# Kernel optimization log

Hardware: AMD Instinct MI355X
Metric: run time of the kernel (lower is better)

## Reference

```python
import jax, jax.numpy as jnp
import numpy as np

N_NODES = 200000
N_EVENTS = 200000
MEM_DIM = 128
MSG_DIM = 128
TIME_DIM = 16
MSG_IN = 2 * MEM_DIM + MSG_DIM + TIME_DIM  # 400


def setup_inputs() -> dict:
    key = jax.random.key(0)
    ks = jax.random.split(key, 12)
    return {
        "src_ids": jax.random.randint(ks[0], (N_EVENTS,), 0, N_NODES, dtype=jnp.int32),
        "dst_ids": jax.random.randint(ks[1], (N_EVENTS,), 0, N_NODES, dtype=jnp.int32),
        "edge_feat": jax.random.normal(ks[2], (N_EVENTS, MSG_DIM), dtype=jnp.float32),
        "timestamps": jax.random.uniform(ks[3], (N_EVENTS,), dtype=jnp.float32),
        "memory": jax.random.normal(ks[4], (N_NODES, MEM_DIM), dtype=jnp.float32) * 0.1,
        "last_update_time": jnp.zeros((N_NODES,), dtype=jnp.float32),
        "time_w": jax.random.normal(ks[5], (TIME_DIM,), dtype=jnp.float32),
        "time_phi": jnp.zeros((TIME_DIM,), dtype=jnp.float32),
        "W1": jax.random.normal(ks[6], (MSG_IN, MSG_DIM), dtype=jnp.float32) / np.sqrt(MSG_IN),
        "b1": jnp.zeros((MSG_DIM,), dtype=jnp.float32),
        "W2": jax.random.normal(ks[7], (MSG_DIM, MSG_DIM), dtype=jnp.float32) / np.sqrt(MSG_DIM),
        "b2": jnp.zeros((MSG_DIM,), dtype=jnp.float32),
        "W_ih": jax.random.normal(ks[8], (3 * MEM_DIM, MSG_DIM), dtype=jnp.float32) / np.sqrt(MSG_DIM),
        "W_hh": jax.random.normal(ks[9], (3 * MEM_DIM, MEM_DIM), dtype=jnp.float32) / np.sqrt(MEM_DIM),
        "b_ih": jnp.zeros((3 * MEM_DIM,), dtype=jnp.float32),
        "b_hh": jnp.zeros((3 * MEM_DIM,), dtype=jnp.float32),
    }


def _time_encode(dt, w, phi):
    # Time2Vec: linear first channel, sin on the rest
    wt = dt[:, None] * w[None, :] + phi[None, :]  # [E, TIME_DIM]
    return jnp.concatenate([wt[:, :1], jnp.sin(wt[:, 1:])], axis=-1)


def _message_mlp(x, W1, b1, W2, b2):
    h = jax.nn.relu(x @ W1 + b1)
    return h @ W2 + b2


def _gru_cell(x, h, W_ih, W_hh, b_ih, b_hh):
    gi = x @ W_ih.T + b_ih  # [U, 3H]
    gh = h @ W_hh.T + b_hh
    i_r, i_z, i_n = jnp.split(gi, 3, axis=-1)
    h_r, h_z, h_n = jnp.split(gh, 3, axis=-1)
    r = jax.nn.sigmoid(i_r + h_r)
    z = jax.nn.sigmoid(i_z + h_z)
    n = jnp.tanh(i_n + r * h_n)
    return (1.0 - z) * n + z * h


def reference(src_ids, dst_ids, edge_feat, timestamps, memory, last_update_time,
              time_w, time_phi, W1, b1, W2, b2, W_ih, W_hh, b_ih, b_hh):
    # 1) gather + time encode
    dt_src = timestamps - last_update_time[src_ids]
    dt_dst = timestamps - last_update_time[dst_ids]
    te_src = _time_encode(dt_src, time_w, time_phi)
    te_dst = _time_encode(dt_dst, time_w, time_phi)
    src_mem = memory[src_ids]
    dst_mem = memory[dst_ids]

    # 2) messages
    msg_src = _message_mlp(jnp.concatenate([src_mem, dst_mem, edge_feat, te_src], -1), W1, b1, W2, b2)
    msg_dst = _message_mlp(jnp.concatenate([dst_mem, src_mem, edge_feat, te_dst], -1), W1, b1, W2, b2)

    all_nodes = jnp.concatenate([src_ids, dst_ids])  # [2E]
    all_msgs = jnp.concatenate([msg_src, msg_dst], axis=0)  # [2E, MSG_DIM]

    # 3) 'last' aggregation: segment-max of positions, then gather
    pos = jnp.arange(all_nodes.shape[0], dtype=jnp.int32)
    last_pos = jax.ops.segment_max(pos, all_nodes, num_segments=N_NODES)  # int32 min where absent
    present = last_pos >= 0  # [N]
    agg = all_msgs[jnp.clip(last_pos, 0, None)]  # [N, MSG_DIM]
    agg = jnp.where(present[:, None], agg, 0.0)

    # 4) GRU memory update on involved nodes only
    new_mem = _gru_cell(agg, memory, W_ih, W_hh, b_ih, b_hh)
    memory_out = jnp.where(present[:, None], new_mem, memory)
    return memory_out
```

## Files before the change

kernel.cpp:

```cpp
#include <hip/hip_runtime.h>
#include <hip/hip_bf16.h>
#include <math.h>

#define NN 200000
#define NE 200000

typedef __attribute__((ext_vector_type(8))) short bf16x8;
typedef __attribute__((ext_vector_type(4))) float f32x4;

#define XASTR 136
#define XBSTR 296
#define OSTR  132
#define NT    (NN / 32)
#define PBT   (32 * XBSTR)

__device__ __forceinline__ float sigm(float x) { return 1.0f / (1.0f + __expf(-x)); }
__device__ __forceinline__ float tanh_f(float x) {
    float e = __expf(2.0f * x);
    return 1.0f - 2.0f / (e + 1.0f);
}
__device__ __forceinline__ ushort f2b(float x) {
    union { __hip_bfloat16 b; ushort u; } v;
    v.b = __float2bfloat16(x);
    return v.u;
}
__device__ __forceinline__ float b2f(ushort u) {
    return __uint_as_float(((unsigned)u) << 16);
}
__device__ __forceinline__ ushort4 cvt4(float4 v) {
    ushort4 u; u.x = f2b(v.x); u.y = f2b(v.y); u.z = f2b(v.z); u.w = f2b(v.w);
    return u;
}
__device__ __forceinline__ void gload_lds16(const ushort* g, ushort* l) {
    __builtin_amdgcn_global_load_lds(
        (const __attribute__((address_space(1))) unsigned int*)g,
        (__attribute__((address_space(3))) unsigned int*)l, 16, 0, 0);
}

#define MFMA16(a, b, c) __builtin_amdgcn_mfma_f32_16x16x32_bf16((a), (b), (c), 0, 0, 0)

#define NB_PREP 594
#define NB_SCAT (((2 * NE) + 255) / 256)
__global__ void k_pre(const float* __restrict__ W1, const float* __restrict__ W2,
                      const float* __restrict__ Wih, const float* __restrict__ Whh,
                      const float* __restrict__ b2, const float* __restrict__ bih,
                      ushort* __restrict__ W1F, ushort* __restrict__ W2IF,
                      ushort* __restrict__ WHF, float* __restrict__ cb,
                      const int* __restrict__ src, const int* __restrict__ dst,
                      int* __restrict__ last_pos) {
    int b = blockIdx.x;
    if (b >= NB_PREP) {
        int i = (b - NB_PREP) * 256 + threadIdx.x;
        if (i < NE) {
            atomicMax(&last_pos[src[i]], i);
        } else if (i < 2 * NE) {
            atomicMax(&last_pos[dst[i - NE]], i);
        }
        return;
    }
    int t = b * 256 + threadIdx.x;
    if (t < 104 * 512) {
        int f = t >> 9, idx = t & 511;
        int lane = idx >> 3, j = idx & 7, c16 = lane & 15, k8 = lane >> 4;
        int wvv = f / 26, r = f % 26, kt = r >> 1, ns = r & 1;
        int col = wvv * 32 + ns * 16 + c16;
        int kk = kt * 32 + k8 * 8 + j;
        W1F[t] = (kk < 400) ? f2b(W1[kk * 128 + col]) : (ushort)0;
        return;
    }
    t -= 104 * 512;
    if (t < 96 * 512) {
        int f = t >> 9, idx = t & 511;
        int lane = idx >> 3, j = idx & 7, c16 = lane & 15, k8 = lane >> 4;
        int wvv = f / 24, r = f % 24, kt = r / 6, rem = r % 6, g = rem >> 1, ns = rem & 1;
        int col = g * 128 + wvv * 32 + ns * 16 + c16;
        int kk = kt * 32 + k8 * 8 + j;
        float s = 0.0f;
        for (int c = 0; c < 128; ++c) s = fmaf(W2[kk * 128 + c], Wih[col * 128 + c], s);
        W2IF[f * 512 + idx] = f2b(s);
        return;
    }
    t -= 96 * 512;
    if (t < 96 * 512) {
        int f = t >> 9, idx = t & 511;
        int lane = idx >> 3, j = idx & 7, c16 = lane & 15, k8 = lane >> 4;
        int wvv = f / 24, r = f % 24, kt = r / 6, rem = r % 6, g = rem >> 1, ns = rem & 1;
        int col = g * 128 + wvv * 32 + ns * 16 + c16;
        int kk = kt * 32 + k8 * 8 + j;
        WHF[f * 512 + idx] = f2b(Whh[col * 128 + kk]);
        return;
    }
    t -= 96 * 512;
    if (t < 384) {
        float s = bih[t];
        for (int k = 0; k < 128; ++k) s = fmaf(b2[k], Wih[t * 128 + k], s);
        cb[t] = s;
    }
}

__global__ __launch_bounds__(256)
void k_gath(const int* __restrict__ last_pos,
            const int* __restrict__ src, const int* __restrict__ dst,
            const float* __restrict__ ts, const float* __restrict__ lut,
            const float* __restrict__ mem, const float* __restrict__ ef,
            const float* __restrict__ tw, const float* __restrict__ tphi,
            ushort* __restrict__ PB)
{
    const int wv = threadIdx.x >> 6, lane = threadIdx.x & 63;
    const int n0 = (blockIdx.x * 4 + wv) * 4;
    const int l = lane & 31;
    const bool lo = lane < 32;

    int p[4];
    #pragma unroll
    for (int s = 0; s < 4; ++s) p[s] = last_pos[n0 + s];

    float4 mv[4], fv[4];
    float te[4];
    #pragma unroll
    for (int s = 0; s < 4; ++s) {
        te[s] = 0.0f;
        if (p[s] >= 0) {
            int e = (p[s] < NE) ? p[s] : p[s] - NE;
            int o = (p[s] < NE) ? dst[e] : src[e];
            if (lo) {
                mv[s] = *(const float4*)&mem[(size_t)o * 128 + l * 4];
                if (l < 16) {
                    float dt = ts[e] - lut[n0 + s];
                    float w = fmaf(dt, tw[l], tphi[l]);
                    te[s] = (l == 0) ? w : __sinf(w);
                }
            } else {
                fv[s] = *(const float4*)&ef[(size_t)e * 128 + l * 4];
            }
        }
    }
    #pragma unroll
    for (int s = 0; s < 4; ++s) {
        if (p[s] >= 0) {
            ushort* xb = PB + (size_t)(n0 + s) * XBSTR;
            if (lo) {
                *(ushort4*)&xb[l * 4] = cvt4(mv[s]);
                xb[256 + l] = (l < 16) ? f2b(te[s]) : (ushort)0;
            } else {
                *(ushort4*)&xb[128 + l * 4] = cvt4(fv[s]);
            }
        }
    }
}

__global__ __launch_bounds__(256, 3)
void k_main8(const ushort* __restrict__ PB, const int* __restrict__ last_pos,
             const float* __restrict__ mem,
             const ushort* __restrict__ W1F, const float* __restrict__ b1,
             const ushort* __restrict__ W2IF, const ushort* __restrict__ WHF,
             const float* __restrict__ cb, const float* __restrict__ bhh,
             float* __restrict__ out)
{
    __shared__ __align__(16) ushort XA[32 * XASTR];
    __shared__ __align__(16) ushort HB[32 * XASTR];
    __shared__ __align__(16) ushort XB[32 * XBSTR];
    __shared__ unsigned char pres[32];

    const int tile = (NT - 1) - blockIdx.x;
    const int base = tile * 32;
    const int tid  = threadIdx.x;
    const int lane = tid & 63;
    const int wv   = tid >> 6;
    const int r16  = lane & 15;
    const int kb   = lane >> 4;

    {
        const ushort* srcPB = PB + (size_t)tile * PBT;
        #pragma unroll
        for (int j = 0; j < 5; ++j) {
            int cc = wv + j * 4;
            if (cc < 18) gload_lds16(srcPB + cc * 512 + lane * 8, XB + cc * 512);
            else if (cc == 18 && lane < 32) gload_lds16(srcPB + cc * 512 + lane * 8, XB + cc * 512);
        }
    }
    {
        const float* msrc = mem + (size_t)base * 128;
        #pragma unroll
        for (int k = 0; k < 4; ++k) {
            int i0 = k * 1024 + tid * 4;
            float4 v = *(const float4*)&msrc[i0];
            *(ushort4*)&XA[(i0 >> 7) * XASTR + (i0 & 127)] = cvt4(v);
        }
        if (tid < 32) pres[tid] = (unsigned char)(last_pos[base + tid] >= 0);
    }
    const ushort* w1 = W1F  + wv * (26 * 512) + lane * 8;
    const ushort* wI = W2IF + wv * (24 * 512) + lane * 8;
    const ushort* wH = WHF  + wv * (24 * 512) + lane * 8;
    __syncthreads();

    f32x4 c1[2][2] = {};
    {
        const ushort* aA = &XA[r16 * XASTR + kb * 8];
        const ushort* aB = &XB[r16 * XBSTR + kb * 8];
        __builtin_amdgcn_s_setprio(1);
        #pragma unroll
        for (int kt = 0; kt < 13; ++kt) {
            const ushort* ap  = (kt < 4) ? (aA + kt * 32) : (aB + (kt - 4) * 32);
            const int     ast = (kt < 4) ? XASTR : XBSTR;
            bf16x8 A0 = *(const bf16x8*)ap;
            bf16x8 A1 = *(const bf16x8*)(ap + 16 * ast);
            bf16x8 B0 = *(const bf16x8*)(w1 + (kt * 2 + 0) * 512);
            bf16x8 B1 = *(const bf16x8*)(w1 + (kt * 2 + 1) * 512);
            c1[0][0] = MFMA16(A0, B0, c1[0][0]);
            c1[0][1] = MFMA16(A0, B1, c1[0][1]);
            c1[1][0] = MFMA16(A1, B0, c1[1][0]);
            c1[1][1] = MFMA16(A1, B1, c1[1][1]);
        }
        __builtin_amdgcn_s_setprio(0);
    }
    #pragma unroll
    for (int ns = 0; ns < 2; ++ns) {
        int col = wv * 32 + ns * 16 + r16;
        float bb = b1[col];
        #pragma unroll
        for (int m = 0; m < 2; ++m)
            #pragma unroll
            for (int r = 0; r < 4; ++r)
                HB[(m * 16 + kb * 4 + r) * XASTR + col] =
                    f2b(fmaxf(c1[m][ns][r] + bb, 0.0f));
    }
    __syncthreads();

    f32x4 arz[2][4] = {};
    f32x4 an_i[2][2] = {};
    f32x4 an_h[2][2] = {};
    {
        const ushort* am = &HB[r16 * XASTR + kb * 8];
        const ushort* ah = &XA[r16 * XASTR + kb * 8];
        __builtin_amdgcn_s_setprio(1);
        #pragma unroll
        for (int kt = 0; kt < 4; ++kt) {
            bf16x8 M0 = *(const bf16x8*)(am + kt * 32);
            bf16x8 M1 = *(const bf16x8*)(am + 16 * XASTR + kt * 32);
            bf16x8 H0 = *(const bf16x8*)(ah + kt * 32);
            bf16x8 H1 = *(const bf16x8*)(ah + 16 * XASTR + kt * 32);
            #pragma unroll
            for (int g = 0; g < 2; ++g)
                #pragma unroll
                for (int ns = 0; ns < 2; ++ns) {
                    int fo = (kt * 6 + g * 2 + ns) * 512;
                    bf16x8 Bi = *(const bf16x8*)(wI + fo);
                    bf16x8 Bh = *(const bf16x8*)(wH + fo);
                    arz[0][g * 2 + ns] = MFMA16(M0, Bi, arz[0][g * 2 + ns]);
                    arz[0][g * 2 + ns] = MFMA16(H0, Bh, arz[0][g * 2 + ns]);
                    arz[1][g * 2 + ns] = MFMA16(M1, Bi, arz[1][g * 2 + ns]);
                    arz[1][g * 2 + ns] = MFMA16(H1, Bh, arz[1][g * 2 + ns]);
                }
            #pragma unroll
            for (int ns = 0; ns < 2; ++ns) {
                int fo = (kt * 6 + 4 + ns) * 512;
                bf16x8 Bi = *(const bf16x8*)(wI + fo);
                bf16x8 Bh = *(const bf16x8*)(wH + fo);
                an_i[0][ns] = MFMA16(M0, Bi, an_i[0][ns]);
                an_i[1][ns] = MFMA16(M1, Bi, an_i[1][ns]);
                an_h[0][ns] = MFMA16(H0, Bh, an_h[0][ns]);
                an_h[1][ns] = MFMA16(H1, Bh, an_h[1][ns]);
            }
        }
        __builtin_amdgcn_s_setprio(0);
    }

    float* XBf = (float*)XB;
    #pragma unroll
    for (int ns = 0; ns < 2; ++ns) {
        int col = wv * 32 + ns * 16 + r16;
        float brz0 = cb[col] + bhh[col];
        float brz1 = cb[128 + col] + bhh[128 + col];
        float bin  = cb[256 + col];
        float bhn  = bhh[256 + col];
        #pragma unroll
        for (int m = 0; m < 2; ++m) {
            #pragma unroll
            for (int r = 0; r < 4; ++r) {
                int row = m * 16 + kb * 4 + r;
                float rr = sigm(arz[m][0 + ns][r] + brz0);
                float zz = sigm(arz[m][2 + ns][r] + brz1);
                float nn = tanh_f(an_i[m][ns][r] + bin +
                                  rr * (an_h[m][ns][r] + bhn));
                float hh = b2f(XA[row * XASTR + col]);
                XBf[row * OSTR + col] = (1.0f - zz) * nn + zz * hh;
            }
        }
    }
    __syncthreads();

    for (int j = wv; j < 32; j += 4) {
        float2 v;
        if (pres[j]) v = *(const float2*)&XBf[j * OSTR + lane * 2];
        else         v = *(const float2*)&mem[(size_t)(base + j) * 128 + lane * 2];
        *(float2*)&out[(size_t)(base + j) * 128 + lane * 2] = v;
    }
}

extern "C" void kernel_launch(void* const* d_in, const int* in_sizes, int n_in,
                              void* d_out, int out_size, void* d_ws, size_t ws_size,
                              hipStream_t stream) {
    const int*   src  = (const int*)d_in[0];
    const int*   dst  = (const int*)d_in[1];
    const float* ef   = (const float*)d_in[2];
    const float* ts   = (const float*)d_in[3];
    const float* mem  = (const float*)d_in[4];
    const float* lut  = (const float*)d_in[5];
    const float* tw   = (const float*)d_in[6];
    const float* tphi = (const float*)d_in[7];
    const float* W1   = (const float*)d_in[8];
    const float* b1   = (const float*)d_in[9];
    const float* W2   = (const float*)d_in[10];
    const float* b2   = (const float*)d_in[11];
    const float* Wih  = (const float*)d_in[12];
    const float* Whh  = (const float*)d_in[13];
    const float* bih  = (const float*)d_in[14];
    const float* bhh  = (const float*)d_in[15];
    float* out = (float*)d_out;

    char* ws = (char*)d_ws;
    size_t off = 0;
    int*    last_pos = (int*)(ws + off);    off += (size_t)NN * 4;
    ushort* W1F      = (ushort*)(ws + off); off += (size_t)104 * 512 * 2;
    ushort* W2IF     = (ushort*)(ws + off); off += (size_t)96 * 512 * 2;
    ushort* WHF      = (ushort*)(ws + off); off += (size_t)96 * 512 * 2;
    float*  cb       = (float*)(ws + off);  off += (size_t)384 * 4 + 64;
    ushort* PB       = (ushort*)(ws + off);

    hipMemsetAsync(last_pos, 0xFF, (size_t)NN * sizeof(int), stream);

    k_pre<<<NB_PREP + NB_SCAT, 256, 0, stream>>>(
        W1, W2, Wih, Whh, b2, bih, W1F, W2IF, WHF, cb, src, dst, last_pos);
    k_gath<<<NN / 16, 256, 0, stream>>>(last_pos, src, dst, ts, lut, mem, ef, tw, tphi, PB);
    k_main8<<<NT, 256, 0, stream>>>(PB, last_pos, mem, W1F, b1, W2IF, WHF, cb, bhh, out);
}
```

Before: 260.3 us.

## Regroup kernels: split scatter out, fuse weight prep with gather, raise occupancy

```diff
diff --git a/kernel.cpp b/kernel.cpp
--- a/kernel.cpp
+++ b/kernel.cpp
@@ -39,75 +39,76 @@
 
 #define MFMA16(a, b, c) __builtin_amdgcn_mfma_f32_16x16x32_bf16((a), (b), (c), 0, 0, 0)
 
+__global__ void k_scatter(const int* __restrict__ src, const int* __restrict__ dst,
+                          int* __restrict__ last_pos) {
+    int i = blockIdx.x * blockDim.x + threadIdx.x;
+    if (i < NE) {
+        atomicMax(&last_pos[src[i]], i);
+    } else if (i < 2 * NE) {
+        atomicMax(&last_pos[dst[i - NE]], i);
+    }
+}
+
 #define NB_PREP 594
-#define NB_SCAT (((2 * NE) + 255) / 256)
-__global__ void k_pre(const float* __restrict__ W1, const float* __restrict__ W2,
-                      const float* __restrict__ Wih, const float* __restrict__ Whh,
-                      const float* __restrict__ b2, const float* __restrict__ bih,
-                      ushort* __restrict__ W1F, ushort* __restrict__ W2IF,
-                      ushort* __restrict__ WHF, float* __restrict__ cb,
-                      const int* __restrict__ src, const int* __restrict__ dst,
-                      int* __restrict__ last_pos) {
+#define NB_GATH (NN / 16)
+__global__ __launch_bounds__(256)
+void k_pg(const float* __restrict__ W1, const float* __restrict__ W2,
+          const float* __restrict__ Wih, const float* __restrict__ Whh,
+          const float* __restrict__ b2, const float* __restrict__ bih,
+          ushort* __restrict__ W1F, ushort* __restrict__ W2IF,
+          ushort* __restrict__ WHF, float* __restrict__ cb,
+          const int* __restrict__ last_pos,
+          const int* __restrict__ src, const int* __restrict__ dst,
+          const float* __restrict__ ts, const float* __restrict__ lut,
+          const float* __restrict__ mem, const float* __restrict__ ef,
+          const float* __restrict__ tw, const float* __restrict__ tphi,
+          ushort* __restrict__ PB)
+{
     int b = blockIdx.x;
-    if (b >= NB_PREP) {
-        int i = (b - NB_PREP) * 256 + threadIdx.x;
-        if (i < NE) {
-            atomicMax(&last_pos[src[i]], i);
-        } else if (i < 2 * NE) {
-            atomicMax(&last_pos[dst[i - NE]], i);
+    if (b < NB_PREP) {
+        int t = b * 256 + threadIdx.x;
+        if (t < 104 * 512) {
+            int f = t >> 9, idx = t & 511;
+            int lane = idx >> 3, j = idx & 7, c16 = lane & 15, k8 = lane >> 4;
+            int wvv = f / 26, r = f % 26, kt = r >> 1, ns = r & 1;
+            int col = wvv * 32 + ns * 16 + c16;
+            int kk = kt * 32 + k8 * 8 + j;
+            W1F[t] = (kk < 400) ? f2b(W1[kk * 128 + col]) : (ushort)0;
+            return;
+        }
+        t -= 104 * 512;
+        if (t < 96 * 512) {
+            int f = t >> 9, idx = t & 511;
+            int lane = idx >> 3, j = idx & 7, c16 = lane & 15, k8 = lane >> 4;
+            int wvv = f / 24, r = f % 24, kt = r / 6, rem = r % 6, g = rem >> 1, ns = rem & 1;
+            int col = g * 128 + wvv * 32 + ns * 16 + c16;
+            int kk = kt * 32 + k8 * 8 + j;
+            float s = 0.0f;
+            for (int c = 0; c < 128; ++c) s = fmaf(W2[kk * 128 + c], Wih[col * 128 + c], s);
+            W2IF[f * 512 + idx] = f2b(s);
+            return;
+        }
+        t -= 96 * 512;
+        if (t < 96 * 512) {
+            int f = t >> 9, idx = t & 511;
+            int lane = idx >> 3, j = idx & 7, c16 = lane & 15, k8 = lane >> 4;
+            int wvv = f / 24, r = f % 24, kt = r / 6, rem = r % 6, g = rem >> 1, ns = rem & 1;
+            int col = g * 128 + wvv * 32 + ns * 16 + c16;
+            int kk = kt * 32 + k8 * 8 + j;
+            WHF[f * 512 + idx] = f2b(Whh[col * 128 + kk]);
+            return;
+        }
+        t -= 96 * 512;
+        if (t < 384) {
+            float s = bih[t];
+            for (int k = 0; k < 128; ++k) s = fmaf(b2[k], Wih[t * 128 + k], s);
+            cb[t] = s;
         }
         return;
     }
-    int t = b * 256 + threadIdx.x;
-    if (t < 104 * 512) {
-        int f = t >> 9, idx = t & 511;
-        int lane = idx >> 3, j = idx & 7, c16 = lane & 15, k8 = lane >> 4;
-        int wvv = f / 26, r = f % 26, kt = r >> 1, ns = r & 1;
-        int col = wvv * 32 + ns * 16 + c16;
-        int kk = kt * 32 + k8 * 8 + j;
-        W1F[t] = (kk < 400) ? f2b(W1[kk * 128 + col]) : (ushort)0;
-        return;
-    }
-    t -= 104 * 512;
-    if (t < 96 * 512) {
-        int f = t >> 9, idx = t & 511;
-        int lane = idx >> 3, j = idx & 7, c16 = lane & 15, k8 = lane >> 4;
-        int wvv = f / 24, r = f % 24, kt = r / 6, rem = r % 6, g = rem >> 1, ns = rem & 1;
-        int col = g * 128 + wvv * 32 + ns * 16 + c16;
-        int kk = kt * 32 + k8 * 8 + j;
-        float s = 0.0f;
-        for (int c = 0; c < 128; ++c) s = fmaf(W2[kk * 128 + c], Wih[col * 128 + c], s);
-        W2IF[f * 512 + idx] = f2b(s);
-        return;
-    }
-    t -= 96 * 512;
-    if (t < 96 * 512) {
-        int f = t >> 9, idx = t & 511;
-        int lane = idx >> 3, j = idx & 7, c16 = lane & 15, k8 = lane >> 4;
-        int wvv = f / 24, r = f % 24, kt = r / 6, rem = r % 6, g = rem >> 1, ns = rem & 1;
-        int col = g * 128 + wvv * 32 + ns * 16 + c16;
-        int kk = kt * 32 + k8 * 8 + j;
-        WHF[f * 512 + idx] = f2b(Whh[col * 128 + kk]);
-        return;
-    }
-    t -= 96 * 512;
-    if (t < 384) {
-        float s = bih[t];
-        for (int k = 0; k < 128; ++k) s = fmaf(b2[k], Wih[t * 128 + k], s);
-        cb[t] = s;
-    }
-}
-
-__global__ __launch_bounds__(256)
-void k_gath(const int* __restrict__ last_pos,
-            const int* __restrict__ src, const int* __restrict__ dst,
-            const float* __restrict__ ts, const float* __restrict__ lut,
-            const float* __restrict__ mem, const float* __restrict__ ef,
-            const float* __restrict__ tw, const float* __restrict__ tphi,
-            ushort* __restrict__ PB)
-{
+
     const int wv = threadIdx.x >> 6, lane = threadIdx.x & 63;
-    const int n0 = (blockIdx.x * 4 + wv) * 4;
+    const int n0 = (((b - NB_PREP) * 4) + wv) * 4;
     const int l = lane & 31;
     const bool lo = lane < 32;
 
@@ -149,8 +150,8 @@
     }
 }
 
-__global__ __launch_bounds__(256, 3)
-void k_main8(const ushort* __restrict__ PB, const int* __restrict__ last_pos,
+__global__ __launch_bounds__(256, 4)
+void k_main9(const ushort* __restrict__ PB, const int* __restrict__ last_pos,
              const float* __restrict__ mem,
              const ushort* __restrict__ W1F, const float* __restrict__ b1,
              const ushort* __restrict__ W2IF, const ushort* __restrict__ WHF,
@@ -198,7 +199,6 @@
     {
         const ushort* aA = &XA[r16 * XASTR + kb * 8];
         const ushort* aB = &XB[r16 * XBSTR + kb * 8];
-        __builtin_amdgcn_s_setprio(1);
         #pragma unroll
         for (int kt = 0; kt < 13; ++kt) {
             const ushort* ap  = (kt < 4) ? (aA + kt * 32) : (aB + (kt - 4) * 32);
@@ -212,7 +212,6 @@
             c1[1][0] = MFMA16(A1, B0, c1[1][0]);
             c1[1][1] = MFMA16(A1, B1, c1[1][1]);
         }
-        __builtin_amdgcn_s_setprio(0);
     }
     #pragma unroll
     for (int ns = 0; ns < 2; ++ns) {
@@ -233,7 +232,6 @@
     {
         const ushort* am = &HB[r16 * XASTR + kb * 8];
         const ushort* ah = &XA[r16 * XASTR + kb * 8];
-        __builtin_amdgcn_s_setprio(1);
         #pragma unroll
         for (int kt = 0; kt < 4; ++kt) {
             bf16x8 M0 = *(const bf16x8*)(am + kt * 32);
@@ -263,7 +261,6 @@
                 an_h[1][ns] = MFMA16(H1, Bh, an_h[1][ns]);
             }
         }
-        __builtin_amdgcn_s_setprio(0);
     }
 
     float* XBf = (float*)XB;
@@ -284,7 +281,7 @@
                 float nn = tanh_f(an_i[m][ns][r] + bin +
                                   rr * (an_h[m][ns][r] + bhn));
                 float hh = b2f(XA[row * XASTR + col]);
-                XBf[row * OSTR + col] = (1.0f - zz) * nn + zz * hh;
+                XBf[row * OSTR + col] = fmaf(zz, hh - nn, nn);
             }
         }
     }
@@ -330,8 +327,9 @@
 
     hipMemsetAsync(last_pos, 0xFF, (size_t)NN * sizeof(int), stream);
 
-    k_pre<<<NB_PREP + NB_SCAT, 256, 0, stream>>>(
-        W1, W2, Wih, Whh, b2, bih, W1F, W2IF, WHF, cb, src, dst, last_pos);
-    k_gath<<<NN / 16, 256, 0, stream>>>(last_pos, src, dst, ts, lut, mem, ef, tw, tphi, PB);
-    k_main8<<<NT, 256, 0, stream>>>(PB, last_pos, mem, W1F, b1, W2IF, WHF, cb, bhh, out);
-}
+    k_scatter<<<(2 * NE + 255) / 256, 256, 0, stream>>>(src, dst, last_pos);
+    k_pg<<<NB_PREP + NB_GATH, 256, 0, stream>>>(
+        W1, W2, Wih, Whh, b2, bih, W1F, W2IF, WHF, cb,
+        last_pos, src, dst, ts, lut, mem, ef, tw, tphi, PB);
+    k_main9<<<NT, 256, 0, stream>>>(PB, last_pos, mem, W1F, b1, W2IF, WHF, cb, bhh, out);
+}
```

Measured after the change: 238.8 us. -8.3%, faster.
